# Kernel optimization log

Measured on AMD Instinct MI355X. Metric: run time of the kernel, lower is better.

Reference implementation:

```python
import jax, jax.numpy as jnp
import numpy as np

EMB = 1024
N_HEADS = 16
HEAD = EMB // N_HEADS
EPS = 1e-5


def layernorm(x, g, b):
    mu = jnp.mean(x, axis=-1, keepdims=True)
    var = jnp.var(x, axis=-1, keepdims=True)
    return (x - mu) * jax.lax.rsqrt(var + EPS) * g + b


def setup_inputs() -> dict:
    key = jax.random.key(0)
    ks = jax.random.split(key, 12)
    s = lambda fan_in: 1.0 / np.sqrt(fan_in)
    return {
        "x": jax.random.normal(ks[0], (8, 1024, EMB), dtype=jnp.float32),
        "ln1_g": jnp.ones((EMB,), jnp.float32),
        "ln1_b": jnp.zeros((EMB,), jnp.float32),
        "wq": jax.random.uniform(ks[1], (EMB, EMB), jnp.float32, -s(EMB), s(EMB)),
        "wk": jax.random.uniform(ks[2], (EMB, EMB), jnp.float32, -s(EMB), s(EMB)),
        "wv": jax.random.uniform(ks[3], (EMB, EMB), jnp.float32, -s(EMB), s(EMB)),
        "w_proj": jax.random.uniform(ks[4], (EMB, EMB), jnp.float32, -s(EMB), s(EMB)),
        "b_proj": jnp.zeros((EMB,), jnp.float32),
        "ln2_g": jnp.ones((EMB,), jnp.float32),
        "ln2_b": jnp.zeros((EMB,), jnp.float32),
        "w1": jax.random.uniform(ks[5], (EMB, 4 * EMB), jnp.float32, -s(EMB), s(EMB)),
        "b1": jnp.zeros((4 * EMB,), jnp.float32),
        "w2": jax.random.uniform(ks[6], (4 * EMB, EMB), jnp.float32, -s(4 * EMB), s(4 * EMB)),
        "b2": jnp.zeros((EMB,), jnp.float32),
    }


def reference(x, ln1_g, ln1_b, wq, wk, wv, w_proj, b_proj, ln2_g, ln2_b, w1, b1, w2, b2):
    B, T, E = x.shape
    h = layernorm(x, ln1_g, ln1_b)
    # per-head no-bias projections == one big matmul then split into heads
    q = (h @ wq).reshape(B, T, N_HEADS, HEAD).transpose(0, 2, 1, 3)  # [B,H,T,D]
    k = (h @ wk).reshape(B, T, N_HEADS, HEAD).transpose(0, 2, 1, 3)
    v = (h @ wv).reshape(B, T, N_HEADS, HEAD).transpose(0, 2, 1, 3)
    scores = jnp.einsum("bhqd,bhkd->bhqk", q, k) * (HEAD ** -0.5)
    causal = jnp.tril(jnp.ones((T, T), dtype=bool))
    scores = jnp.where(causal, scores, -jnp.inf)
    wei = jax.nn.softmax(scores, axis=-1)  # dropout is identity at eval
    attn = jnp.einsum("bhqk,bhkd->bhqd", wei, v)
    attn = attn.transpose(0, 2, 1, 3).reshape(B, T, E)
    out = x + attn @ w_proj + b_proj
    h2 = layernorm(out, ln2_g, ln2_b)
    mlp = jax.nn.gelu(h2 @ w1 + b1, approximate=False) @ w2 + b2
    return out + mlp
```

## Files before the change

### kernel.cpp

```cpp
#include <hip/hip_runtime.h>
#include <hip/hip_bf16.h>

#define EMB 1024
#define NH 16
#define HD 64
#define BATCH 8
#define SEQ 1024
#define ROWS (BATCH*SEQ)
#define MT (ROWS/128)

typedef unsigned short ushort_t;
typedef __attribute__((ext_vector_type(8))) short bf16x8;
typedef __attribute__((ext_vector_type(4))) float f32x4;
typedef __attribute__((ext_vector_type(16))) float f32x16;

__device__ __forceinline__ float bf2f(ushort_t u){
    union { unsigned int i; float f; } v; v.i = ((unsigned int)u) << 16; return v.f;
}
__device__ __forceinline__ ushort_t f2bf(float f){
    unsigned int u = __float_as_uint(f);
    unsigned int r = (u + 0x7FFFu + ((u >> 16) & 1u)) >> 16;
    return (ushort_t)r;
}
__device__ __forceinline__ void gload16(const ushort_t* g, ushort_t* l){
    __builtin_amdgcn_global_load_lds(
        (const __attribute__((address_space(1))) void*)g,
        (__attribute__((address_space(3))) void*)l,
        16, 0, 0);
}
__device__ __forceinline__ float gelu_f(float v){
    float x = fabsf(v) * 0.70710678118654752f;
    float t = __builtin_amdgcn_rcpf(1.0f + 0.3275911f * x);
    float poly = t*(0.254829592f + t*(-0.284496736f + t*(1.421413741f + t*(-1.453152027f + t*1.061405429f))));
    float erfa = 1.0f - poly * __expf(-x*x);
    float erfv = (v >= 0.f) ? erfa : -erfa;
    return 0.5f * v * (1.0f + erfv);
}

__global__ __launch_bounds__(256) void transpose_w(const float* __restrict__ in,
                                                   ushort_t* __restrict__ out,
                                                   int K, int N){
    __shared__ ushort_t t[32][33];
    int tx = threadIdx.x & 31, ty = threadIdx.x >> 5;
    int bx = blockIdx.x, by = blockIdx.y;
    #pragma unroll
    for (int r = 0; r < 4; ++r)
        t[ty + r*8][tx] = f2bf(in[(size_t)(by*32 + ty + r*8) * N + bx*32 + tx]);
    __syncthreads();
    #pragma unroll
    for (int r = 0; r < 4; ++r)
        out[(size_t)(bx*32 + ty + r*8) * K + by*32 + tx] = t[tx][ty + r*8];
}

__global__ __launch_bounds__(256) void ln_kernel(const float* __restrict__ xin,
                                                 const float* __restrict__ g,
                                                 const float* __restrict__ bia,
                                                 ushort_t* __restrict__ out){
    int row = blockIdx.x;
    int tid = threadIdx.x;
    const float* x = xin + (size_t)row * EMB;
    float4 f = *(const float4*)(x + tid*4);
    float v[4] = {f.x, f.y, f.z, f.w};
    float s = v[0]+v[1]+v[2]+v[3];
    float q = v[0]*v[0]+v[1]*v[1]+v[2]*v[2]+v[3]*v[3];
    #pragma unroll
    for (int o = 32; o > 0; o >>= 1){ s += __shfl_down(s, o); q += __shfl_down(q, o); }
    __shared__ float ss[4], qq[4];
    __shared__ float mu_s, sc_s;
    int wave = tid >> 6, lane = tid & 63;
    if (lane == 0){ ss[wave] = s; qq[wave] = q; }
    __syncthreads();
    if (tid == 0){
        float S = ss[0]+ss[1]+ss[2]+ss[3];
        float Q = qq[0]+qq[1]+qq[2]+qq[3];
        float mu = S * (1.0f/EMB);
        float var = Q * (1.0f/EMB) - mu*mu;
        mu_s = mu; sc_s = rsqrtf(var + 1e-5f);
    }
    __syncthreads();
    float mu = mu_s, sc = sc_s;
    float4 gu = *(const float4*)(g + tid*4);
    float4 bu = *(const float4*)(bia + tid*4);
    ushort4 o4;
    o4.x = f2bf((v[0]-mu)*sc*gu.x + bu.x);
    o4.y = f2bf((v[1]-mu)*sc*gu.y + bu.y);
    o4.z = f2bf((v[2]-mu)*sc*gu.z + bu.z);
    o4.w = f2bf((v[3]-mu)*sc*gu.w + bu.w);
    *(ushort4*)(out + (size_t)row*EMB + tid*4) = o4;
}

template<int MODE>
__global__ __launch_bounds__(256) void gemm_kernel(const ushort_t* __restrict__ A,
                                                   const ushort_t* __restrict__ Bt,
                                                   const float* __restrict__ bias,
                                                   const float* __restrict__ resid,
                                                   void* __restrict__ out,
                                                   int M, int N, int K){
    __shared__ ushort_t As[128*64];
    __shared__ ushort_t Bs[128*64];
    int tid = threadIdx.x;
    int lane = tid & 63, wave = tid >> 6;
    int l31 = lane & 31, half = lane >> 5;
    int wm = wave >> 1, wn = wave & 1;
    int bid = blockIdx.x;
    int m0 = (bid & (MT-1)) * 128, n0 = (bid >> 6) * 128;

    f32x16 acc[2][2];
    #pragma unroll
    for (int i=0;i<2;i++)
        #pragma unroll
        for (int j=0;j<2;j++)
            #pragma unroll
            for (int r=0;r<16;r++) acc[i][j][r] = 0.f;

    int lr  = lane >> 3;
    int lch = lane & 7;
    const ushort_t* gA = A  + (size_t)(m0 + wave*32 + lr)*K + (lch ^ lr)*8;
    const ushort_t* gB = Bt + (size_t)(n0 + wave*32 + lr)*K + (lch ^ lr)*8;
    ushort_t* lA = &As[(wave*32)*64];
    ushort_t* lB = &Bs[(wave*32)*64];
    int sx = lane & 7;

    for (int k0 = 0; k0 < K; k0 += 64){
        #pragma unroll
        for (int i = 0; i < 4; ++i){
            gload16(gA + (size_t)(i*8)*K + k0, lA + i*8*64);
            gload16(gB + (size_t)(i*8)*K + k0, lB + i*8*64);
        }
        __syncthreads();
        #pragma unroll
        for (int s = 0; s < 4; ++s){
            int ch = ((s<<1) | half) ^ sx;
            bf16x8 af[2], bfr[2];
            #pragma unroll
            for (int i=0;i<2;i++) af[i]  = *(const bf16x8*)&As[(wm*64 + i*32 + l31)*64 + ch*8];
            #pragma unroll
            for (int j=0;j<2;j++) bfr[j] = *(const bf16x8*)&Bs[(wn*64 + j*32 + l31)*64 + ch*8];
            #pragma unroll
            for (int i=0;i<2;i++)
                #pragma unroll
                for (int j=0;j<2;j++)
                    acc[i][j] = __builtin_amdgcn_mfma_f32_32x32x16_bf16(af[i], bfr[j], acc[i][j], 0,0,0);
        }
        __syncthreads();
    }

    int rowoff = 4*half;
    #pragma unroll
    for (int i=0;i<2;i++){
        #pragma unroll
        for (int j=0;j<2;j++){
            int n = n0 + wn*64 + j*32 + l31;
            #pragma unroll
            for (int reg=0; reg<16; ++reg){
                int m = m0 + wm*64 + i*32 + (reg&3) + 8*(reg>>2) + rowoff;
                float v = acc[i][j][reg];
                size_t idx = (size_t)m*N + n;
                if (MODE == 0){
                    ((ushort_t*)out)[idx] = f2bf(v);
                } else if (MODE == 1){
                    v += bias[n] + resid[idx];
                    ((float*)out)[idx] = v;
                } else if (MODE == 2){
                    v += bias[n];
                    ((ushort_t*)out)[idx] = f2bf(gelu_f(v));
                } else {
                    v += bias[n] + resid[idx];
                    ((float*)out)[idx] = v;
                }
            }
        }
    }
}

__global__ __launch_bounds__(256) void attn_kernel(const ushort_t* __restrict__ qkv,
                                                   ushort_t* __restrict__ attn_out){
    __shared__ ushort_t Qs[128][72];
    __shared__ ushort_t Ks[64][72];
    __shared__ ushort_t Vts[64][72];
    __shared__ ushort_t Ps[128][72];

    int tid = threadIdx.x;
    int lane = tid & 63, wave = tid >> 6;
    int quad = lane >> 4, l15 = lane & 15;
    int pair = blockIdx.x;
    int bh = blockIdx.y;
    int b = bh >> 4, h = bh & 15;
    size_t tb = (size_t)b * SEQ;

    int tr = tid >> 3;
    int tc = (tid & 7) * 8;
    int sw_w = tid & 7;

    for (int t = 0; t < 2; ++t){
        int qi = t ? (7 - pair) : pair;

        #pragma unroll
        for (int p = 0; p < 4; ++p){
            int r = tr + p*32;
            size_t tok = tb + qi*128 + r;
            *(bf16x8*)&Qs[r][tc] = *(const bf16x8*)(qkv + tok*3072 + h*64 + tc);
        }

        f32x4 o_acc[2][4];
        #pragma unroll
        for (int mt=0;mt<2;mt++)
            #pragma unroll
            for (int nt=0;nt<4;nt++) o_acc[mt][nt] = (f32x4){0.f,0.f,0.f,0.f};
        float m_st[2][4], l_st[2][4];
        #pragma unroll
        for (int mt=0;mt<2;mt++)
            #pragma unroll
            for (int r=0;r<4;r++){ m_st[mt][r] = -1e30f; l_st[mt][r] = 0.f; }

        int nj = 2*qi + 2;
        for (int j = 0; j < nj; ++j){
            #pragma unroll
            for (int p = 0; p < 2; ++p){
                int r = tr + p*32;
                size_t tok = tb + j*64 + r;
                *(bf16x8*)&Ks[r][tc] = *(const bf16x8*)(qkv + tok*3072 + 1024 + h*64 + tc);
                bf16x8 vv = *(const bf16x8*)(qkv + tok*3072 + 2048 + h*64 + tc);
                int kcol = r ^ (sw_w << 3);
                #pragma unroll
                for (int c = 0; c < 8; ++c) Vts[tc + c][kcol] = (ushort_t)vv[c];
            }
            __syncthreads();

            f32x4 s_acc[2][4];
            #pragma unroll
            for (int mt=0;mt<2;mt++)
                #pragma unroll
                for (int nt=0;nt<4;nt++) s_acc[mt][nt] = (f32x4){0.f,0.f,0.f,0.f};
            #pragma unroll
            for (int kf = 0; kf < 2; ++kf){
                bf16x8 aq[2], bk[4];
                #pragma unroll
                for (int mt=0;mt<2;mt++) aq[mt] = *(const bf16x8*)&Qs[wave*32 + mt*16 + l15][kf*32 + quad*8];
                #pragma unroll
                for (int nt=0;nt<4;nt++) bk[nt] = *(const bf16x8*)&Ks[nt*16 + l15][kf*32 + quad*8];
                #pragma unroll
                for (int mt=0;mt<2;mt++)
                    #pragma unroll
                    for (int nt=0;nt<4;nt++)
                        s_acc[mt][nt] = __builtin_amdgcn_mfma_f32_16x16x32_bf16(aq[mt], bk[nt], s_acc[mt][nt], 0,0,0);
            }

            bool need_mask = (j >= 2*qi);
            #pragma unroll
            for (int mt=0;mt<2;mt++)
                #pragma unroll
                for (int nt=0;nt<4;nt++)
                    #pragma unroll
                    for (int r=0;r<4;r++){
                        float s = s_acc[mt][nt][r] * 0.125f;
                        if (need_mask){
                            int qg = qi*128 + wave*32 + mt*16 + quad*4 + r;
                            int kg = j*64 + nt*16 + l15;
                            if (kg > qg) s = -1e30f;
                        }
                        s_acc[mt][nt][r] = s;
                    }

            #pragma unroll
            for (int mt=0;mt<2;mt++){
                #pragma unroll
                for (int r=0;r<4;r++){
                    float rm = s_acc[mt][0][r];
                    #pragma unroll
                    for (int nt=1;nt<4;nt++) rm = fmaxf(rm, s_acc[mt][nt][r]);
                    rm = fmaxf(rm, __shfl_xor(rm, 1));
                    rm = fmaxf(rm, __shfl_xor(rm, 2));
                    rm = fmaxf(rm, __shfl_xor(rm, 4));
                    rm = fmaxf(rm, __shfl_xor(rm, 8));
                    float mnew = fmaxf(m_st[mt][r], rm);
                    float alpha = __expf(m_st[mt][r] - mnew);
                    float rsum = 0.f;
                    #pragma unroll
                    for (int nt=0;nt<4;nt++){
                        float p = __expf(s_acc[mt][nt][r] - mnew);
                        s_acc[mt][nt][r] = p;
                        rsum += p;
                    }
                    rsum += __shfl_xor(rsum, 1);
                    rsum += __shfl_xor(rsum, 2);
                    rsum += __shfl_xor(rsum, 4);
                    rsum += __shfl_xor(rsum, 8);
                    l_st[mt][r] = l_st[mt][r]*alpha + rsum;
                    m_st[mt][r] = mnew;
                    #pragma unroll
                    for (int nt=0;nt<4;nt++) o_acc[mt][nt][r] *= alpha;
                }
            }

            #pragma unroll
            for (int mt=0;mt<2;mt++)
                #pragma unroll
                for (int nt=0;nt<4;nt++)
                    #pragma unroll
                    for (int r=0;r<4;r++)
                        Ps[wave*32 + mt*16 + quad*4 + r][nt*16 + l15] = f2bf(s_acc[mt][nt][r]);

            #pragma unroll
            for (int kf = 0; kf < 2; ++kf){
                bf16x8 ap[2], bv[4];
                #pragma unroll
                for (int mt=0;mt<2;mt++) ap[mt] = *(const bf16x8*)&Ps[wave*32 + mt*16 + l15][kf*32 + quad*8];
                #pragma unroll
                for (int nt=0;nt<4;nt++){
                    int d = nt*16 + l15;
                    int col = (kf*32 + quad*8) ^ (((d >> 3) & 7) << 3);
                    bv[nt] = *(const bf16x8*)&Vts[d][col];
                }
                #pragma unroll
                for (int mt=0;mt<2;mt++)
                    #pragma unroll
                    for (int nt=0;nt<4;nt++)
                        o_acc[mt][nt] = __builtin_amdgcn_mfma_f32_16x16x32_bf16(ap[mt], bv[nt], o_acc[mt][nt], 0,0,0);
            }
            __syncthreads();
        }

        #pragma unroll
        for (int mt=0;mt<2;mt++)
            #pragma unroll
            for (int r=0;r<4;r++){
                float inv = 1.0f / l_st[mt][r];
                size_t tok = tb + qi*128 + wave*32 + mt*16 + quad*4 + r;
                #pragma unroll
                for (int nt=0;nt<4;nt++)
                    attn_out[tok*EMB + h*64 + nt*16 + l15] = f2bf(o_acc[mt][nt][r] * inv);
            }
    }
}

extern "C" void kernel_launch(void* const* d_in, const int* in_sizes, int n_in,
                              void* d_out, int out_size, void* d_ws, size_t ws_size,
                              hipStream_t stream){
    const float* x      = (const float*)d_in[0];
    const float* ln1_g  = (const float*)d_in[1];
    const float* ln1_b  = (const float*)d_in[2];
    const float* wq     = (const float*)d_in[3];
    const float* wk     = (const float*)d_in[4];
    const float* wv     = (const float*)d_in[5];
    const float* w_proj = (const float*)d_in[6];
    const float* b_proj = (const float*)d_in[7];
    const float* ln2_g  = (const float*)d_in[8];
    const float* ln2_b  = (const float*)d_in[9];
    const float* w1     = (const float*)d_in[10];
    const float* b1     = (const float*)d_in[11];
    const float* w2     = (const float*)d_in[12];
    const float* b2     = (const float*)d_in[13];
    float* outp = (float*)d_out;

    char* ws = (char*)d_ws;
    size_t off = 0;
    auto alloc = [&](size_t bytes)->char*{ char* p = ws + off; off += (bytes + 255) & ~255ULL; return p; };
    ushort_t* wqkv_t = (ushort_t*)alloc((size_t)3072*1024*2);
    ushort_t* wproj_t= (ushort_t*)alloc((size_t)1024*1024*2);
    ushort_t* w1_t   = (ushort_t*)alloc((size_t)4096*1024*2);
    ushort_t* w2_t   = (ushort_t*)alloc((size_t)1024*4096*2);
    ushort_t* qkv    = (ushort_t*)alloc((size_t)ROWS*3072*2);
    ushort_t* hbuf   = (ushort_t*)alloc((size_t)ROWS*1024*2);
    float*    out32  = (float*)  alloc((size_t)ROWS*1024*4);
    ushort_t* mid    = (ushort_t*)alloc((size_t)ROWS*4096*2);
    ushort_t* h1 = hbuf;
    ushort_t* attn = hbuf;
    ushort_t* h2 = qkv;

    dim3 blk(256);
    transpose_w<<<dim3(32,32),  blk, 0, stream>>>(wq,     wqkv_t,               1024, 1024);
    transpose_w<<<dim3(32,32),  blk, 0, stream>>>(wk,     wqkv_t + 1024*1024,   1024, 1024);
    transpose_w<<<dim3(32,32),  blk, 0, stream>>>(wv,     wqkv_t + 2*1024*1024, 1024, 1024);
    transpose_w<<<dim3(32,32),  blk, 0, stream>>>(w_proj, wproj_t,              1024, 1024);
    transpose_w<<<dim3(128,32), blk, 0, stream>>>(w1,     w1_t,                 1024, 4096);
    transpose_w<<<dim3(32,128), blk, 0, stream>>>(w2,     w2_t,                 4096, 1024);

    ln_kernel<<<ROWS, blk, 0, stream>>>(x, ln1_g, ln1_b, h1);
    gemm_kernel<0><<<dim3(MT*(3072/128)), blk, 0, stream>>>(h1, wqkv_t, nullptr, nullptr, qkv, ROWS, 3072, 1024);
    attn_kernel<<<dim3(4,128), blk, 0, stream>>>(qkv, attn);
    gemm_kernel<1><<<dim3(MT*(1024/128)), blk, 0, stream>>>(attn, wproj_t, b_proj, x, out32, ROWS, 1024, 1024);
    ln_kernel<<<ROWS, blk, 0, stream>>>(out32, ln2_g, ln2_b, h2);
    gemm_kernel<2><<<dim3(MT*(4096/128)), blk, 0, stream>>>(h2, w1_t, b1, nullptr, mid, ROWS, 4096, 1024);
    gemm_kernel<3><<<dim3(MT*(1024/128)), blk, 0, stream>>>(mid, w2_t, b2, out32, outp, ROWS, 1024, 4096);
}
```

Before: 489.5 us.

## Transpose attention MFMA so softmax rows live per-lane, use swizzled LDS and async loads

Rewrites the attention kernel to compute S^T = K·Q^T, so each lane holds a whole query column. Row max and sum then need only two cross-lane shuffles instead of four per row, and P can be stored to LDS as packed 4-element vectors. Q and K are loaded with gload16 (likely direct global-to-LDS copies) into XOR-swizzled unpadded tiles, which saves LDS and avoids bank conflicts. Output stores become 4-wide vectors. The cost is more intricate indexing, with correctness depending on the swizzle and the mask transposition being right.

```diff
diff --git a/kernel.cpp b/kernel.cpp
--- a/kernel.cpp
+++ b/kernel.cpp
@@ -175,10 +175,10 @@
 
 __global__ __launch_bounds__(256) void attn_kernel(const ushort_t* __restrict__ qkv,
                                                    ushort_t* __restrict__ attn_out){
-    __shared__ ushort_t Qs[128][72];
-    __shared__ ushort_t Ks[64][72];
+    __shared__ ushort_t Qs[128*64];
+    __shared__ ushort_t Ks[64*64];
     __shared__ ushort_t Vts[64][72];
-    __shared__ ushort_t Ps[128][72];
+    __shared__ ushort_t Ps[128*64];
 
     int tid = threadIdx.x;
     int lane = tid & 63, wave = tid >> 6;
@@ -188,149 +188,158 @@
     int b = bh >> 4, h = bh & 15;
     size_t tb = (size_t)b * SEQ;
 
+    int lr = lane >> 3, lch = lane & 7;
     int tr = tid >> 3;
     int tc = (tid & 7) * 8;
     int sw_w = tid & 7;
+    int sx = l15 & 7;
 
     for (int t = 0; t < 2; ++t){
         int qi = t ? (7 - pair) : pair;
 
-        #pragma unroll
-        for (int p = 0; p < 4; ++p){
-            int r = tr + p*32;
-            size_t tok = tb + qi*128 + r;
-            *(bf16x8*)&Qs[r][tc] = *(const bf16x8*)(qkv + tok*3072 + h*64 + tc);
-        }
-
-        f32x4 o_acc[2][4];
-        #pragma unroll
-        for (int mt=0;mt<2;mt++)
-            #pragma unroll
-            for (int nt=0;nt<4;nt++) o_acc[mt][nt] = (f32x4){0.f,0.f,0.f,0.f};
-        float m_st[2][4], l_st[2][4];
-        #pragma unroll
-        for (int mt=0;mt<2;mt++)
-            #pragma unroll
-            for (int r=0;r<4;r++){ m_st[mt][r] = -1e30f; l_st[mt][r] = 0.f; }
+        {
+            const ushort_t* gq = qkv + (size_t)(tb + qi*128 + wave*32 + lr)*3072 + h*64 + (lch^lr)*8;
+            ushort_t* lq = &Qs[(wave*32)*64];
+            #pragma unroll
+            for (int p = 0; p < 4; ++p)
+                gload16(gq + (size_t)(p*8)*3072, lq + p*8*64);
+        }
+
+        f32x4 o_acc[4][2];
+        #pragma unroll
+        for (int i=0;i<4;i++)
+            #pragma unroll
+            for (int j=0;j<2;j++) o_acc[i][j] = (f32x4){0.f,0.f,0.f,0.f};
+        float m_st[2] = {-1e30f, -1e30f};
+        float l_st[2] = {0.f, 0.f};
 
         int nj = 2*qi + 2;
         for (int j = 0; j < nj; ++j){
+            {
+                const ushort_t* gk = qkv + (size_t)(tb + j*64 + wave*16 + lr)*3072 + 1024 + h*64 + (lch^lr)*8;
+                ushort_t* lk = &Ks[(wave*16)*64];
+                gload16(gk, lk);
+                gload16(gk + (size_t)8*3072, lk + 8*64);
+            }
             #pragma unroll
             for (int p = 0; p < 2; ++p){
                 int r = tr + p*32;
-                size_t tok = tb + j*64 + r;
-                *(bf16x8*)&Ks[r][tc] = *(const bf16x8*)(qkv + tok*3072 + 1024 + h*64 + tc);
-                bf16x8 vv = *(const bf16x8*)(qkv + tok*3072 + 2048 + h*64 + tc);
+                bf16x8 vv = *(const bf16x8*)(qkv + (size_t)(tb + j*64 + r)*3072 + 2048 + h*64 + tc);
                 int kcol = r ^ (sw_w << 3);
                 #pragma unroll
                 for (int c = 0; c < 8; ++c) Vts[tc + c][kcol] = (ushort_t)vv[c];
             }
             __syncthreads();
 
-            f32x4 s_acc[2][4];
-            #pragma unroll
-            for (int mt=0;mt<2;mt++)
-                #pragma unroll
-                for (int nt=0;nt<4;nt++) s_acc[mt][nt] = (f32x4){0.f,0.f,0.f,0.f};
+            f32x4 st[4][2];
+            #pragma unroll
+            for (int mt=0;mt<4;mt++)
+                #pragma unroll
+                for (int nt=0;nt<2;nt++) st[mt][nt] = (f32x4){0.f,0.f,0.f,0.f};
             #pragma unroll
             for (int kf = 0; kf < 2; ++kf){
-                bf16x8 aq[2], bk[4];
-                #pragma unroll
-                for (int mt=0;mt<2;mt++) aq[mt] = *(const bf16x8*)&Qs[wave*32 + mt*16 + l15][kf*32 + quad*8];
-                #pragma unroll
-                for (int nt=0;nt<4;nt++) bk[nt] = *(const bf16x8*)&Ks[nt*16 + l15][kf*32 + quad*8];
-                #pragma unroll
-                for (int mt=0;mt<2;mt++)
-                    #pragma unroll
-                    for (int nt=0;nt<4;nt++)
-                        s_acc[mt][nt] = __builtin_amdgcn_mfma_f32_16x16x32_bf16(aq[mt], bk[nt], s_acc[mt][nt], 0,0,0);
+                int ch = (kf*4 + quad) ^ sx;
+                bf16x8 ak[4], bq[2];
+                #pragma unroll
+                for (int mt=0;mt<4;mt++) ak[mt] = *(const bf16x8*)&Ks[(mt*16 + l15)*64 + ch*8];
+                #pragma unroll
+                for (int nt=0;nt<2;nt++) bq[nt] = *(const bf16x8*)&Qs[(wave*32 + nt*16 + l15)*64 + ch*8];
+                #pragma unroll
+                for (int mt=0;mt<4;mt++)
+                    #pragma unroll
+                    for (int nt=0;nt<2;nt++)
+                        st[mt][nt] = __builtin_amdgcn_mfma_f32_16x16x32_bf16(ak[mt], bq[nt], st[mt][nt], 0,0,0);
             }
 
             bool need_mask = (j >= 2*qi);
             #pragma unroll
-            for (int mt=0;mt<2;mt++)
-                #pragma unroll
-                for (int nt=0;nt<4;nt++)
+            for (int mt=0;mt<4;mt++)
+                #pragma unroll
+                for (int nt=0;nt<2;nt++)
                     #pragma unroll
                     for (int r=0;r<4;r++){
-                        float s = s_acc[mt][nt][r] * 0.125f;
+                        float s = st[mt][nt][r] * 0.125f;
                         if (need_mask){
-                            int qg = qi*128 + wave*32 + mt*16 + quad*4 + r;
-                            int kg = j*64 + nt*16 + l15;
+                            int kg = j*64 + mt*16 + quad*4 + r;
+                            int qg = qi*128 + wave*32 + nt*16 + l15;
                             if (kg > qg) s = -1e30f;
                         }
-                        s_acc[mt][nt][r] = s;
+                        st[mt][nt][r] = s;
                     }
 
             #pragma unroll
-            for (int mt=0;mt<2;mt++){
-                #pragma unroll
-                for (int r=0;r<4;r++){
-                    float rm = s_acc[mt][0][r];
-                    #pragma unroll
-                    for (int nt=1;nt<4;nt++) rm = fmaxf(rm, s_acc[mt][nt][r]);
-                    rm = fmaxf(rm, __shfl_xor(rm, 1));
-                    rm = fmaxf(rm, __shfl_xor(rm, 2));
-                    rm = fmaxf(rm, __shfl_xor(rm, 4));
-                    rm = fmaxf(rm, __shfl_xor(rm, 8));
-                    float mnew = fmaxf(m_st[mt][r], rm);
-                    float alpha = __expf(m_st[mt][r] - mnew);
-                    float rsum = 0.f;
-                    #pragma unroll
-                    for (int nt=0;nt<4;nt++){
-                        float p = __expf(s_acc[mt][nt][r] - mnew);
-                        s_acc[mt][nt][r] = p;
-                        rsum += p;
+            for (int nt = 0; nt < 2; ++nt){
+                float mx = st[0][nt][0];
+                #pragma unroll
+                for (int mt=0;mt<4;mt++)
+                    #pragma unroll
+                    for (int r=0;r<4;r++) mx = fmaxf(mx, st[mt][nt][r]);
+                mx = fmaxf(mx, __shfl_xor(mx, 16));
+                mx = fmaxf(mx, __shfl_xor(mx, 32));
+                float mnew = fmaxf(m_st[nt], mx);
+                float al = __expf(m_st[nt] - mnew);
+                float ps = 0.f;
+                #pragma unroll
+                for (int mt=0;mt<4;mt++)
+                    #pragma unroll
+                    for (int r=0;r<4;r++){
+                        float p = __expf(st[mt][nt][r] - mnew);
+                        st[mt][nt][r] = p;
+                        ps += p;
                     }
-                    rsum += __shfl_xor(rsum, 1);
-                    rsum += __shfl_xor(rsum, 2);
-                    rsum += __shfl_xor(rsum, 4);
-                    rsum += __shfl_xor(rsum, 8);
-                    l_st[mt][r] = l_st[mt][r]*alpha + rsum;
-                    m_st[mt][r] = mnew;
-                    #pragma unroll
-                    for (int nt=0;nt<4;nt++) o_acc[mt][nt][r] *= alpha;
+                ps += __shfl_xor(ps, 16);
+                ps += __shfl_xor(ps, 32);
+                l_st[nt] = l_st[nt]*al + ps;
+                m_st[nt] = mnew;
+                #pragma unroll
+                for (int mtd=0;mtd<4;mtd++)
+                    #pragma unroll
+                    for (int r=0;r<4;r++) o_acc[mtd][nt][r] *= al;
+                #pragma unroll
+                for (int mt=0;mt<4;mt++){
+                    int slot = (mt*2 + (quad>>1)) ^ sx;
+                    ushort4 pk;
+                    pk.x = f2bf(st[mt][nt][0]); pk.y = f2bf(st[mt][nt][1]);
+                    pk.z = f2bf(st[mt][nt][2]); pk.w = f2bf(st[mt][nt][3]);
+                    *(ushort4*)&Ps[(wave*32 + nt*16 + l15)*64 + slot*8 + (quad&1)*4] = pk;
                 }
             }
 
             #pragma unroll
-            for (int mt=0;mt<2;mt++)
-                #pragma unroll
-                for (int nt=0;nt<4;nt++)
-                    #pragma unroll
-                    for (int r=0;r<4;r++)
-                        Ps[wave*32 + mt*16 + quad*4 + r][nt*16 + l15] = f2bf(s_acc[mt][nt][r]);
-
-            #pragma unroll
             for (int kf = 0; kf < 2; ++kf){
-                bf16x8 ap[2], bv[4];
-                #pragma unroll
-                for (int mt=0;mt<2;mt++) ap[mt] = *(const bf16x8*)&Ps[wave*32 + mt*16 + l15][kf*32 + quad*8];
-                #pragma unroll
-                for (int nt=0;nt<4;nt++){
-                    int d = nt*16 + l15;
+                bf16x8 av[4], bp[2];
+                #pragma unroll
+                for (int mtd=0;mtd<4;mtd++){
+                    int d = mtd*16 + l15;
                     int col = (kf*32 + quad*8) ^ (((d >> 3) & 7) << 3);
-                    bv[nt] = *(const bf16x8*)&Vts[d][col];
+                    av[mtd] = *(const bf16x8*)&Vts[d][col];
                 }
                 #pragma unroll
-                for (int mt=0;mt<2;mt++)
-                    #pragma unroll
-                    for (int nt=0;nt<4;nt++)
-                        o_acc[mt][nt] = __builtin_amdgcn_mfma_f32_16x16x32_bf16(ap[mt], bv[nt], o_acc[mt][nt], 0,0,0);
+                for (int nt=0;nt<2;nt++){
+                    int ch = (kf*4 + quad) ^ sx;
+                    bp[nt] = *(const bf16x8*)&Ps[(wave*32 + nt*16 + l15)*64 + ch*8];
+                }
+                #pragma unroll
+                for (int mtd=0;mtd<4;mtd++)
+                    #pragma unroll
+                    for (int nt=0;nt<2;nt++)
+                        o_acc[mtd][nt] = __builtin_amdgcn_mfma_f32_16x16x32_bf16(av[mtd], bp[nt], o_acc[mtd][nt], 0,0,0);
             }
             __syncthreads();
         }
 
         #pragma unroll
-        for (int mt=0;mt<2;mt++)
-            #pragma unroll
-            for (int r=0;r<4;r++){
-                float inv = 1.0f / l_st[mt][r];
-                size_t tok = tb + qi*128 + wave*32 + mt*16 + quad*4 + r;
-                #pragma unroll
-                for (int nt=0;nt<4;nt++)
-                    attn_out[tok*EMB + h*64 + nt*16 + l15] = f2bf(o_acc[mt][nt][r] * inv);
-            }
+        for (int nt = 0; nt < 2; ++nt){
+            float inv = 1.0f / l_st[nt];
+            size_t tok = tb + qi*128 + wave*32 + nt*16 + l15;
+            #pragma unroll
+            for (int mtd = 0; mtd < 4; ++mtd){
+                ushort4 ok;
+                ok.x = f2bf(o_acc[mtd][nt][0]*inv); ok.y = f2bf(o_acc[mtd][nt][1]*inv);
+                ok.z = f2bf(o_acc[mtd][nt][2]*inv); ok.w = f2bf(o_acc[mtd][nt][3]*inv);
+                *(ushort4*)(attn_out + tok*EMB + h*64 + mtd*16 + quad*4) = ok;
+            }
+        }
     }
 }
 
```

After: 463.5 us. -5.3%, faster.
